# Optimization experiments

Measured on AMD Instinct MI355X. Metric: run time of the kernel, lower is better.

Reference implementation:

```python
import jax, jax.numpy as jnp
import numpy as np

N = 10000
E = 160000
DIMS = [256, 256, 256, 256]
EPS = 1e-5
DSCALE = 1.0
SPE_IDX = 0


def setup_inputs() -> dict:
    key = jax.random.key(0)
    ks = jax.random.split(key, 40)
    inp = {}
    inp['x'] = jax.random.normal(ks[0], (N, DIMS[0]), dtype=jnp.float32)
    inp['src'] = jax.random.randint(ks[1], (E,), 0, N, dtype=jnp.int32)
    inp['dst'] = jax.random.randint(ks[2], (E,), 0, N, dtype=jnp.int32)
    k = 3
    for i, (din, dout) in enumerate(zip(DIMS[:-1], DIMS[1:])):
        s = 1.0 / np.sqrt(din)
        inp[f'Ws{i}'] = jax.random.uniform(ks[k], (din, dout), jnp.float32, -s, s); k += 1
        inp[f'Wn{i}'] = jax.random.uniform(ks[k], (din, dout), jnp.float32, -s, s); k += 1
        inp[f'b{i}'] = jnp.zeros((dout,), jnp.float32)
        inp[f'g{i}'] = jnp.ones((dout,), jnp.float32)
        inp[f'be{i}'] = jnp.zeros((dout,), jnp.float32)
    return inp


def _sage(h, src, dst, Ws, Wn, b):
    # mean aggregation over in-neighbors: segment-sum gathered src feats over dst
    agg = jax.ops.segment_sum(h[src], dst, num_segments=N)          # [N, din]
    deg = jax.ops.segment_sum(jnp.ones((E,), h.dtype), dst, num_segments=N)
    mean = agg / jnp.maximum(deg, 1.0)[:, None]
    return h @ Ws + mean @ Wn + b


def _bn(h, g, be):
    # BatchNorm1d, training mode (biased batch variance)
    mu = jnp.mean(h, axis=0)
    var = jnp.mean((h - mu) ** 2, axis=0)
    return (h - mu) * jax.lax.rsqrt(var + EPS) * g + be


def reference(x, src, dst, Ws0, Wn0, b0, g0, be0, Ws1, Wn1, b1, g1, be1,
              Ws2, Wn2, b2, g2, be2):
    params = [(Ws0, Wn0, b0, g0, be0), (Ws1, Wn1, b1, g1, be1),
              (Ws2, Wn2, b2, g2, be2)]
    n_layers = len(params)
    outs = x
    for i, (Ws, Wn, b, g, be) in enumerate(params):
        outs = _sage(outs, src, dst, Ws, Wn, b)
        # hid side-outputs (sigmoid(outs*dscale)[spe_idx]) don't affect outs path
        outs = _bn(outs, g, be)
        if i != n_layers - 1:
            outs = jax.nn.relu(outs)
        else:
            outs = jax.nn.sigmoid(outs)
    return outs
```

## Files before the change

### kernel.cpp

```cpp
#include <hip/hip_runtime.h>
#include <math.h>

#define NN 10000
#define EE 160000
#define DIM 256
#define KK 512
#define CAP 64
#define EPS_BN 1e-5f
#define AST 516

typedef __attribute__((ext_vector_type(8)))  short bf16x8;
typedef __attribute__((ext_vector_type(16))) float f32x16;

union U16 { uint2 u2[2]; bf16x8 v; };

static __device__ __forceinline__ unsigned short f2bf(float f) {
    unsigned u = __float_as_uint(f);
    unsigned r = (u + 0x7fffu + ((u >> 16) & 1u)) >> 16;
    return (unsigned short)r;
}
static __device__ __forceinline__ float bflo(unsigned v) { return __uint_as_float(v << 16); }
static __device__ __forceinline__ float bfhi(unsigned v) { return __uint_as_float(v & 0xffff0000u); }
static __device__ __forceinline__ unsigned packbf(float a, float b) {
    return (unsigned)f2bf(a) | ((unsigned)f2bf(b) << 16);
}

struct Params {
    const float* x; const int* src; const int* dst;
    const float *Ws0, *Wn0, *Ws1, *Wn1, *Ws2, *Wn2;
    const float *g0, *be0, *g1, *be1, *g2, *be2;
    float* out;
    unsigned short* hx;
    unsigned short* z0;
    unsigned short* z1;
    unsigned short* hn;
    unsigned short* magg;
    unsigned short* wcat;
    float* stats;
    int* cnt;
    int* slots;
};

static __device__ __forceinline__ void accum8(float* a, uint4 v) {
    a[0] += bflo(v.x); a[1] += bfhi(v.x);
    a[2] += bflo(v.y); a[3] += bfhi(v.y);
    a[4] += bflo(v.z); a[5] += bfhi(v.z);
    a[6] += bflo(v.w); a[7] += bfhi(v.w);
}

__global__ __launch_bounds__(256) void k_prep(Params P) {
    int g0 = blockIdx.x * 256 + threadIdx.x;
    int stride = gridDim.x * 256;
    for (int g = g0; g < NN * 64; g += stride) {
        int r = g >> 6, c4 = (g & 63) * 4;
        float4 v = *(const float4*)(P.x + (size_t)r * DIM + c4);
        uint2 p; p.x = packbf(v.x, v.y); p.y = packbf(v.z, v.w);
        *(uint2*)(P.hx + (size_t)r * DIM + c4) = p;
    }
    for (int g = g0; g < 3 * DIM * KK; g += stride) {
        int L = g >> 17; int i = g & 131071;
        int k = i >> 8, n = i & 255;
        const float* Ws = (L == 0) ? P.Ws0 : ((L == 1) ? P.Ws1 : P.Ws2);
        const float* Wn = (L == 0) ? P.Wn0 : ((L == 1) ? P.Wn1 : P.Wn2);
        float v = (k < DIM) ? Ws[(size_t)k * DIM + n] : Wn[(size_t)(k - DIM) * DIM + n];
        P.wcat[(size_t)L * DIM * KK + (size_t)n * KK + k] = f2bf(v);
    }
    for (int g = g0; g < NN + 6 * DIM; g += stride) {
        if (g < NN) P.cnt[g] = 0;
        else P.stats[g - NN] = 0.f;
    }
}

__global__ __launch_bounds__(256) void k_bucket(Params P) {
    int e = blockIdx.x * 256 + threadIdx.x;
    if (e < EE) {
        int d = P.dst[e];
        int p = atomicAdd(&P.cnt[d], 1);
        if (p < CAP) P.slots[(size_t)d * CAP + p] = P.src[e];
    }
}

__global__ __launch_bounds__(256) void k_pre(Params P, int Lprev,
                                             const unsigned short* __restrict__ z,
                                             unsigned short* __restrict__ hn) {
    const float* st  = P.stats + Lprev * 2 * DIM;
    const float* gam = (Lprev == 0) ? P.g0 : P.g1;
    const float* bet = (Lprev == 0) ? P.be0 : P.be1;
    int t = threadIdx.x;
    int c8 = (t & 31) * 8;
    int r = blockIdx.x * 8 + (t >> 5);
    float sc[8], sh[8];
#pragma unroll
    for (int i = 0; i < 8; ++i) {
        int c = c8 + i;
        float mu  = st[c] * (1.0f / NN);
        float var = st[DIM + c] * (1.0f / NN) - mu * mu;
        float k = rsqrtf(var + EPS_BN) * gam[c];
        sc[i] = k;
        sh[i] = bet[c] - mu * k;
    }
    uint4 v = *(const uint4*)(z + (size_t)r * DIM + c8);
    uint4 o;
    o.x = packbf(fmaxf(bflo(v.x) * sc[0] + sh[0], 0.f),
                 fmaxf(bfhi(v.x) * sc[1] + sh[1], 0.f));
    o.y = packbf(fmaxf(bflo(v.y) * sc[2] + sh[2], 0.f),
                 fmaxf(bfhi(v.y) * sc[3] + sh[3], 0.f));
    o.z = packbf(fmaxf(bflo(v.z) * sc[4] + sh[4], 0.f),
                 fmaxf(bfhi(v.z) * sc[5] + sh[5], 0.f));
    o.w = packbf(fmaxf(bflo(v.w) * sc[6] + sh[6], 0.f),
                 fmaxf(bfhi(v.w) * sc[7] + sh[7], 0.f));
    *(uint4*)(hn + (size_t)r * DIM + c8) = o;
}

__global__ __launch_bounds__(256) void k_gather(Params P,
                                                const unsigned short* __restrict__ hsrc,
                                                unsigned short* __restrict__ magg) {
    int t = threadIdx.x;
    int wave = t >> 6, lane = t & 63;
    int h = lane >> 5, l = lane & 31;
    int node = blockIdx.x * 4 + wave;
    if (node >= NN) return;
    int cnt = P.cnt[node]; if (cnt > CAP) cnt = CAP;
    int sv = P.slots[(size_t)node * CAP + lane];
    const uint4* srcm = (const uint4*)hsrc;
    float a[8] = {0, 0, 0, 0, 0, 0, 0, 0};
    int j = 0;
    for (; j + 15 < cnt; j += 16) {
        int r0 = __shfl(sv, j +  0 + h), r1 = __shfl(sv, j +  2 + h);
        int r2 = __shfl(sv, j +  4 + h), r3 = __shfl(sv, j +  6 + h);
        int r4 = __shfl(sv, j +  8 + h), r5 = __shfl(sv, j + 10 + h);
        int r6 = __shfl(sv, j + 12 + h), r7 = __shfl(sv, j + 14 + h);
        uint4 v0 = srcm[(size_t)r0 * 32 + l];
        uint4 v1 = srcm[(size_t)r1 * 32 + l];
        uint4 v2 = srcm[(size_t)r2 * 32 + l];
        uint4 v3 = srcm[(size_t)r3 * 32 + l];
        uint4 v4 = srcm[(size_t)r4 * 32 + l];
        uint4 v5 = srcm[(size_t)r5 * 32 + l];
        uint4 v6 = srcm[(size_t)r6 * 32 + l];
        uint4 v7 = srcm[(size_t)r7 * 32 + l];
        accum8(a, v0); accum8(a, v1); accum8(a, v2); accum8(a, v3);
        accum8(a, v4); accum8(a, v5); accum8(a, v6); accum8(a, v7);
    }
    for (; j + 3 < cnt; j += 4) {
        int r0 = __shfl(sv, j + h), r1 = __shfl(sv, j + 2 + h);
        uint4 v0 = srcm[(size_t)r0 * 32 + l];
        uint4 v1 = srcm[(size_t)r1 * 32 + l];
        accum8(a, v0); accum8(a, v1);
    }
    for (; j + 1 < cnt; j += 2) {
        int r0 = __shfl(sv, j + h);
        uint4 v0 = srcm[(size_t)r0 * 32 + l];
        accum8(a, v0);
    }
    if (j < cnt) {
        int r0 = __shfl(sv, cnt - 1);
        uint4 v0 = srcm[(size_t)r0 * 32 + l];
        if (h == 0) accum8(a, v0);
    }
#pragma unroll
    for (int q = 0; q < 8; ++q) a[q] += __shfl_xor(a[q], 32);
    if (h == 0) {
        float inv = 1.0f / (float)(cnt > 1 ? cnt : 1);
        uint4 o;
        o.x = packbf(a[0] * inv, a[1] * inv);
        o.y = packbf(a[2] * inv, a[3] * inv);
        o.z = packbf(a[4] * inv, a[5] * inv);
        o.w = packbf(a[6] * inv, a[7] * inv);
        ((uint4*)magg)[(size_t)node * 32 + l] = o;
    }
}

__global__ __launch_bounds__(512) void k_gemm(Params P, int L,
                                              const unsigned short* __restrict__ hsrc,
                                              const unsigned short* __restrict__ magg,
                                              unsigned short* __restrict__ gdst) {
    __shared__ unsigned short At[32][AST];
    int t = threadIdx.x;
    int wave = t >> 6, lane = t & 63;
    int h = lane >> 5, l = lane & 31;

    {
        int r = t >> 4, q = t & 15;
        int node = blockIdx.x * 32 + r;
        const unsigned short* srcp = (q < 8) ? hsrc : magg;
        int c0 = (q & 7) * 32;
        unsigned short* dstp = &At[r][(q < 8 ? 0 : 256) + c0];
        if (node < NN) {
            const uint4* gp = (const uint4*)(srcp + (size_t)node * DIM + c0);
            uint4 v0 = gp[0], v1 = gp[1], v2 = gp[2], v3 = gp[3];
            *(uint2*)(dstp)      = make_uint2(v0.x, v0.y);
            *(uint2*)(dstp + 4)  = make_uint2(v0.z, v0.w);
            *(uint2*)(dstp + 8)  = make_uint2(v1.x, v1.y);
            *(uint2*)(dstp + 12) = make_uint2(v1.z, v1.w);
            *(uint2*)(dstp + 16) = make_uint2(v2.x, v2.y);
            *(uint2*)(dstp + 20) = make_uint2(v2.z, v2.w);
            *(uint2*)(dstp + 24) = make_uint2(v3.x, v3.y);
            *(uint2*)(dstp + 28) = make_uint2(v3.z, v3.w);
        } else {
            uint2 z = make_uint2(0u, 0u);
#pragma unroll
            for (int q8 = 0; q8 < 8; ++q8) *(uint2*)(dstp + q8 * 4) = z;
        }
    }
    __syncthreads();

    const unsigned short* wcatL = P.wcat + (size_t)L * DIM * KK;
    float* statsL = P.stats + L * 2 * DIM;
    int m = l;
    int row0 = blockIdx.x * 32;
    int colw0 = wave * 32;
    const unsigned short* Bp = wcatL + (size_t)(colw0 + m) * KK + h * 8;
    const unsigned short* Arow = &At[m][0];
    f32x16 acc;
#pragma unroll
    for (int i = 0; i < 16; ++i) acc[i] = 0.f;
#pragma unroll 8
    for (int k0 = 0; k0 < KK; k0 += 16) {
        U16 ua;
        ua.u2[0] = *(const uint2*)(Arow + k0 + h * 8);
        ua.u2[1] = *(const uint2*)(Arow + k0 + h * 8 + 4);
        bf16x8 av = ua.v;
        bf16x8 bv = *(const bf16x8*)(Bp + k0);
        acc = __builtin_amdgcn_mfma_f32_32x32x16_bf16(av, bv, acc, 0, 0, 0);
    }
    int cc = colw0 + m;
    float s = 0.f, s2 = 0.f;
#pragma unroll
    for (int reg = 0; reg < 16; ++reg) {
        int r = row0 + (reg & 3) + 8 * (reg >> 2) + 4 * h;
        if (r < NN) {
            float v = acc[reg];
            gdst[(size_t)r * DIM + cc] = f2bf(v);
            s += v; s2 += v * v;
        }
    }
    s  += __shfl_down(s, 32);
    s2 += __shfl_down(s2, 32);
    if (h == 0) {
        atomicAdd(&statsL[cc], s);
        atomicAdd(&statsL[DIM + cc], s2);
    }
}

__global__ __launch_bounds__(256) void k_norm(Params P) {
    const float* statsL = P.stats + 2 * 2 * DIM;
    int t = threadIdx.x;
    int c8 = (t & 31) * 8;
    int r = blockIdx.x * 8 + (t >> 5);
    float sc[8], sh[8];
#pragma unroll
    for (int i = 0; i < 8; ++i) {
        int c = c8 + i;
        float mu  = statsL[c] * (1.0f / NN);
        float var = statsL[DIM + c] * (1.0f / NN) - mu * mu;
        float k = rsqrtf(var + EPS_BN) * P.g2[c];
        sc[i] = k;
        sh[i] = P.be2[c] - mu * k;
    }
    uint4 v = *(const uint4*)(P.z0 + (size_t)r * DIM + c8);
    float f[8] = {bflo(v.x), bfhi(v.x), bflo(v.y), bfhi(v.y),
                  bflo(v.z), bfhi(v.z), bflo(v.w), bfhi(v.w)};
#pragma unroll
    for (int i = 0; i < 8; ++i) f[i] = f[i] * sc[i] + sh[i];
    float4 o0, o1;
    o0.x = 1.0f / (1.0f + __expf(-f[0]));
    o0.y = 1.0f / (1.0f + __expf(-f[1]));
    o0.z = 1.0f / (1.0f + __expf(-f[2]));
    o0.w = 1.0f / (1.0f + __expf(-f[3]));
    o1.x = 1.0f / (1.0f + __expf(-f[4]));
    o1.y = 1.0f / (1.0f + __expf(-f[5]));
    o1.z = 1.0f / (1.0f + __expf(-f[6]));
    o1.w = 1.0f / (1.0f + __expf(-f[7]));
    *(float4*)(P.out + (size_t)r * DIM + c8)     = o0;
    *(float4*)(P.out + (size_t)r * DIM + c8 + 4) = o1;
}

extern "C" void kernel_launch(void* const* d_in, const int* in_sizes, int n_in,
                              void* d_out, int out_size, void* d_ws, size_t ws_size,
                              hipStream_t stream) {
    Params P;
    P.x   = (const float*)d_in[0];
    P.src = (const int*)d_in[1];
    P.dst = (const int*)d_in[2];
    P.Ws0 = (const float*)d_in[3];  P.Wn0 = (const float*)d_in[4];
    P.g0  = (const float*)d_in[6];  P.be0 = (const float*)d_in[7];
    P.Ws1 = (const float*)d_in[8];  P.Wn1 = (const float*)d_in[9];
    P.g1  = (const float*)d_in[11]; P.be1 = (const float*)d_in[12];
    P.Ws2 = (const float*)d_in[13]; P.Wn2 = (const float*)d_in[14];
    P.g2  = (const float*)d_in[16]; P.be2 = (const float*)d_in[17];
    P.out = (float*)d_out;

    char* ws = (char*)d_ws;
    size_t off = 0;
    P.hx   = (unsigned short*)(ws + off); off += (size_t)NN * DIM * 2;
    P.z0   = (unsigned short*)(ws + off); off += (size_t)NN * DIM * 2;
    P.z1   = (unsigned short*)(ws + off); off += (size_t)NN * DIM * 2;
    P.hn   = (unsigned short*)(ws + off); off += (size_t)NN * DIM * 2;
    P.magg = (unsigned short*)(ws + off); off += (size_t)NN * DIM * 2;
    P.wcat = (unsigned short*)(ws + off); off += (size_t)3 * DIM * KK * 2;
    P.stats = (float*)(ws + off); off += 3 * 2 * DIM * sizeof(float);
    P.cnt   = (int*)(ws + off); off += (size_t)NN * 4; off = (off + 255) & ~(size_t)255;
    P.slots = (int*)(ws + off); off += (size_t)NN * CAP * 4;
    (void)ws_size;

    k_prep<<<512, 256, 0, stream>>>(P);
    k_bucket<<<(EE + 255) / 256, 256, 0, stream>>>(P);
    k_gather<<<2500, 256, 0, stream>>>(P, P.hx, P.magg);
    k_gemm<<<313, 512, 0, stream>>>(P, 0, P.hx, P.magg, P.z0);
    k_pre<<<1250, 256, 0, stream>>>(P, 0, P.z0, P.hn);
    k_gather<<<2500, 256, 0, stream>>>(P, P.hn, P.magg);
    k_gemm<<<313, 512, 0, stream>>>(P, 1, P.hn, P.magg, P.z1);
    k_pre<<<1250, 256, 0, stream>>>(P, 1, P.z1, P.hn);
    k_gather<<<2500, 256, 0, stream>>>(P, P.hn, P.magg);
    k_gemm<<<313, 512, 0, stream>>>(P, 2, P.hn, P.magg, P.z0);
    k_norm<<<NN / 8, 256, 0, stream>>>(P);
}
```

Measured before the change: 220.0 us.

## Split gather feature columns across two blocks, four edges per wave iteration

Each node's 256-wide bf16 feature row is now split into two halves handled by different blocks. Each wave processes four neighbor edges at once in 16-lane groups instead of two edges in 32-lane groups. The grid doubles, and block IDs are interleaved so that both halves of a node group launch close together. This aims to expose more independent gathers and memory parallelism per wave for the mean aggregation, at the cost of duplicated slot and count loads and an extra shuffle-reduction step.

```diff
diff --git a/kernel.cpp b/kernel.cpp
--- a/kernel.cpp
+++ b/kernel.cpp
@@ -117,56 +117,54 @@
                                                 unsigned short* __restrict__ magg) {
     int t = threadIdx.x;
     int wave = t >> 6, lane = t & 63;
-    int h = lane >> 5, l = lane & 31;
-    int node = blockIdx.x * 4 + wave;
+    int g16 = lane >> 4, l16 = lane & 15;
+    int bid = blockIdx.x;
+    int half = (bid >> 2) & 1;
+    int grp  = (bid >> 3) * 4 + (bid & 3);
+    int node = grp * 4 + wave;
     if (node >= NN) return;
     int cnt = P.cnt[node]; if (cnt > CAP) cnt = CAP;
     int sv = P.slots[(size_t)node * CAP + lane];
     const uint4* srcm = (const uint4*)hsrc;
+    int cbase = half * 16 + l16;
     float a[8] = {0, 0, 0, 0, 0, 0, 0, 0};
     int j = 0;
     for (; j + 15 < cnt; j += 16) {
-        int r0 = __shfl(sv, j +  0 + h), r1 = __shfl(sv, j +  2 + h);
-        int r2 = __shfl(sv, j +  4 + h), r3 = __shfl(sv, j +  6 + h);
-        int r4 = __shfl(sv, j +  8 + h), r5 = __shfl(sv, j + 10 + h);
-        int r6 = __shfl(sv, j + 12 + h), r7 = __shfl(sv, j + 14 + h);
-        uint4 v0 = srcm[(size_t)r0 * 32 + l];
-        uint4 v1 = srcm[(size_t)r1 * 32 + l];
-        uint4 v2 = srcm[(size_t)r2 * 32 + l];
-        uint4 v3 = srcm[(size_t)r3 * 32 + l];
-        uint4 v4 = srcm[(size_t)r4 * 32 + l];
-        uint4 v5 = srcm[(size_t)r5 * 32 + l];
-        uint4 v6 = srcm[(size_t)r6 * 32 + l];
-        uint4 v7 = srcm[(size_t)r7 * 32 + l];
+        int r0 = __shfl(sv, j +  0 + g16);
+        int r1 = __shfl(sv, j +  4 + g16);
+        int r2 = __shfl(sv, j +  8 + g16);
+        int r3 = __shfl(sv, j + 12 + g16);
+        uint4 v0 = srcm[(size_t)r0 * 32 + cbase];
+        uint4 v1 = srcm[(size_t)r1 * 32 + cbase];
+        uint4 v2 = srcm[(size_t)r2 * 32 + cbase];
+        uint4 v3 = srcm[(size_t)r3 * 32 + cbase];
         accum8(a, v0); accum8(a, v1); accum8(a, v2); accum8(a, v3);
-        accum8(a, v4); accum8(a, v5); accum8(a, v6); accum8(a, v7);
     }
     for (; j + 3 < cnt; j += 4) {
-        int r0 = __shfl(sv, j + h), r1 = __shfl(sv, j + 2 + h);
-        uint4 v0 = srcm[(size_t)r0 * 32 + l];
-        uint4 v1 = srcm[(size_t)r1 * 32 + l];
-        accum8(a, v0); accum8(a, v1);
-    }
-    for (; j + 1 < cnt; j += 2) {
-        int r0 = __shfl(sv, j + h);
-        uint4 v0 = srcm[(size_t)r0 * 32 + l];
+        int r0 = __shfl(sv, j + g16);
+        uint4 v0 = srcm[(size_t)r0 * 32 + cbase];
         accum8(a, v0);
     }
     if (j < cnt) {
-        int r0 = __shfl(sv, cnt - 1);
-        uint4 v0 = srcm[(size_t)r0 * 32 + l];
-        if (h == 0) accum8(a, v0);
-    }
-#pragma unroll
-    for (int q = 0; q < 8; ++q) a[q] += __shfl_xor(a[q], 32);
-    if (h == 0) {
+        int jj = j + g16;
+        int jc = (jj < cnt) ? jj : j;
+        int r0 = __shfl(sv, jc);
+        uint4 v0 = srcm[(size_t)r0 * 32 + cbase];
+        if (jj < cnt) accum8(a, v0);
+    }
+#pragma unroll
+    for (int q = 0; q < 8; ++q) {
+        a[q] += __shfl_xor(a[q], 16);
+        a[q] += __shfl_xor(a[q], 32);
+    }
+    if (g16 == 0) {
         float inv = 1.0f / (float)(cnt > 1 ? cnt : 1);
         uint4 o;
         o.x = packbf(a[0] * inv, a[1] * inv);
         o.y = packbf(a[2] * inv, a[3] * inv);
         o.z = packbf(a[4] * inv, a[5] * inv);
         o.w = packbf(a[6] * inv, a[7] * inv);
-        ((uint4*)magg)[(size_t)node * 32 + l] = o;
+        ((uint4*)magg)[(size_t)node * 32 + cbase] = o;
     }
 }
 
@@ -305,13 +303,13 @@
 
     k_prep<<<512, 256, 0, stream>>>(P);
     k_bucket<<<(EE + 255) / 256, 256, 0, stream>>>(P);
-    k_gather<<<2500, 256, 0, stream>>>(P, P.hx, P.magg);
+    k_gather<<<5000, 256, 0, stream>>>(P, P.hx, P.magg);
     k_gemm<<<313, 512, 0, stream>>>(P, 0, P.hx, P.magg, P.z0);
     k_pre<<<1250, 256, 0, stream>>>(P, 0, P.z0, P.hn);
-    k_gather<<<2500, 256, 0, stream>>>(P, P.hn, P.magg);
+    k_gather<<<5000, 256, 0, stream>>>(P, P.hn, P.magg);
     k_gemm<<<313, 512, 0, stream>>>(P, 1, P.hn, P.magg, P.z1);
     k_pre<<<1250, 256, 0, stream>>>(P, 1, P.z1, P.hn);
-    k_gather<<<2500, 256, 0, stream>>>(P, P.hn, P.magg);
+    k_gather<<<5000, 256, 0, stream>>>(P, P.hn, P.magg);
     k_gemm<<<313, 512, 0, stream>>>(P, 2, P.hn, P.magg, P.z0);
     k_norm<<<NN / 8, 256, 0, stream>>>(P);
 }
```

Result: no change. 220.9 us (+0.4%).

## Fuse all GraphSAGE layers into one cooperative persistent kernel with grid syncs

Applied to the files above, without the earlier changes.

Replaces the eleven-kernel launch chain with a single cooperative kernel that runs prep, bucketing, gather, GEMM and final norm, separated by grid-wide syncs. The previous layer's BatchNorm and ReLU are now applied on the fly during the gather and when the GEMM A tile is loaded, so the separate pre-normalization pass and its intermediate buffer are gone. The aim is to cut launch gaps and one full read/write of activations per layer. In exchange, the GEMM runs on a grid of 256 or 512 blocks instead of 313, normalization arithmetic is recomputed for every gathered edge, and grid-sync costs are added. The old multi-kernel path remains as a fallback if the cooperative launch fails.

```diff
diff --git a/kernel.cpp b/kernel.cpp
--- a/kernel.cpp
+++ b/kernel.cpp
@@ -1,5 +1,8 @@
 #include <hip/hip_runtime.h>
+#include <hip/hip_cooperative_groups.h>
 #include <math.h>
+
+namespace cg = cooperative_groups;
 
 #define NN 10000
 #define EE 160000
@@ -8,6 +11,7 @@
 #define CAP 64
 #define EPS_BN 1e-5f
 #define AST 516
+#define BLK 512
 
 typedef __attribute__((ext_vector_type(8)))  short bf16x8;
 typedef __attribute__((ext_vector_type(16))) float f32x16;
@@ -46,6 +50,255 @@
     a[2] += bflo(v.y); a[3] += bfhi(v.y);
     a[4] += bflo(v.z); a[5] += bfhi(v.z);
     a[6] += bflo(v.w); a[7] += bfhi(v.w);
+}
+static __device__ __forceinline__ void accum8n(float* a, uint4 v,
+                                               const float* sc, const float* sh) {
+    a[0] += fmaxf(bflo(v.x) * sc[0] + sh[0], 0.f);
+    a[1] += fmaxf(bfhi(v.x) * sc[1] + sh[1], 0.f);
+    a[2] += fmaxf(bflo(v.y) * sc[2] + sh[2], 0.f);
+    a[3] += fmaxf(bfhi(v.y) * sc[3] + sh[3], 0.f);
+    a[4] += fmaxf(bflo(v.z) * sc[4] + sh[4], 0.f);
+    a[5] += fmaxf(bfhi(v.z) * sc[5] + sh[5], 0.f);
+    a[6] += fmaxf(bflo(v.w) * sc[6] + sh[6], 0.f);
+    a[7] += fmaxf(bfhi(v.w) * sc[7] + sh[7], 0.f);
+}
+
+__global__ __launch_bounds__(BLK, 4) void k_mega(Params P) {
+    cg::grid_group grid = cg::this_grid();
+    __shared__ unsigned short At[32][AST];
+    const int t = threadIdx.x;
+    const int bid = blockIdx.x;
+    const int nblk = gridDim.x;
+    const int gtid = bid * BLK + t;
+    const int gstride = nblk * BLK;
+    const int wave = t >> 6, lane = t & 63;
+    const int h = lane >> 5, l = lane & 31;
+
+    for (int g = gtid; g < NN * 64; g += gstride) {
+        int r = g >> 6, c4 = (g & 63) * 4;
+        float4 v = *(const float4*)(P.x + (size_t)r * DIM + c4);
+        uint2 p; p.x = packbf(v.x, v.y); p.y = packbf(v.z, v.w);
+        *(uint2*)(P.hx + (size_t)r * DIM + c4) = p;
+    }
+    for (int g = gtid; g < 3 * DIM * KK; g += gstride) {
+        int L = g >> 17; int i = g & 131071;
+        int k = i >> 8, n = i & 255;
+        const float* Ws = (L == 0) ? P.Ws0 : ((L == 1) ? P.Ws1 : P.Ws2);
+        const float* Wn = (L == 0) ? P.Wn0 : ((L == 1) ? P.Wn1 : P.Wn2);
+        float v = (k < DIM) ? Ws[(size_t)k * DIM + n] : Wn[(size_t)(k - DIM) * DIM + n];
+        P.wcat[(size_t)L * DIM * KK + (size_t)n * KK + k] = f2bf(v);
+    }
+    for (int g = gtid; g < NN + 6 * DIM; g += gstride) {
+        if (g < NN) P.cnt[g] = 0;
+        else P.stats[g - NN] = 0.f;
+    }
+    grid.sync();
+
+    for (int e = gtid; e < EE; e += gstride) {
+        int d = P.dst[e];
+        int p = atomicAdd(&P.cnt[d], 1);
+        if (p < CAP) P.slots[(size_t)d * CAP + p] = P.src[e];
+    }
+    grid.sync();
+
+    for (int L = 0; L < 3; ++L) {
+        const unsigned short* src = (L == 0) ? P.hx : ((L == 1) ? P.z0 : P.z1);
+        unsigned short* dst = (L == 0) ? P.z0 : ((L == 1) ? P.z1 : P.z0);
+        const float* gam = (L == 1) ? P.g0 : P.g1;
+        const float* bet = (L == 1) ? P.be0 : P.be1;
+        const float* stp = P.stats + (L - 1) * 2 * DIM;
+
+        float sc[8], sh[8];
+        if (L > 0) {
+#pragma unroll
+            for (int i = 0; i < 8; ++i) {
+                int c = l * 8 + i;
+                float mu  = stp[c] * (1.0f / NN);
+                float var = stp[DIM + c] * (1.0f / NN) - mu * mu;
+                float k = rsqrtf(var + EPS_BN) * gam[c];
+                sc[i] = k;
+                sh[i] = bet[c] - mu * k;
+            }
+        }
+
+        {
+            const uint4* srcm = (const uint4*)src;
+            int wid = bid * 8 + wave;
+            for (int node = wid; node < NN; node += nblk * 8) {
+                int cnt = P.cnt[node]; if (cnt > CAP) cnt = CAP;
+                int sv = P.slots[(size_t)node * CAP + lane];
+                float a[8] = {0, 0, 0, 0, 0, 0, 0, 0};
+                int j = 0;
+                for (; j + 15 < cnt; j += 16) {
+                    int r0 = __shfl(sv, j +  0 + h), r1 = __shfl(sv, j +  2 + h);
+                    int r2 = __shfl(sv, j +  4 + h), r3 = __shfl(sv, j +  6 + h);
+                    int r4 = __shfl(sv, j +  8 + h), r5 = __shfl(sv, j + 10 + h);
+                    int r6 = __shfl(sv, j + 12 + h), r7 = __shfl(sv, j + 14 + h);
+                    uint4 v0 = srcm[(size_t)r0 * 32 + l];
+                    uint4 v1 = srcm[(size_t)r1 * 32 + l];
+                    uint4 v2 = srcm[(size_t)r2 * 32 + l];
+                    uint4 v3 = srcm[(size_t)r3 * 32 + l];
+                    uint4 v4 = srcm[(size_t)r4 * 32 + l];
+                    uint4 v5 = srcm[(size_t)r5 * 32 + l];
+                    uint4 v6 = srcm[(size_t)r6 * 32 + l];
+                    uint4 v7 = srcm[(size_t)r7 * 32 + l];
+                    if (L == 0) {
+                        accum8(a, v0); accum8(a, v1); accum8(a, v2); accum8(a, v3);
+                        accum8(a, v4); accum8(a, v5); accum8(a, v6); accum8(a, v7);
+                    } else {
+                        accum8n(a, v0, sc, sh); accum8n(a, v1, sc, sh);
+                        accum8n(a, v2, sc, sh); accum8n(a, v3, sc, sh);
+                        accum8n(a, v4, sc, sh); accum8n(a, v5, sc, sh);
+                        accum8n(a, v6, sc, sh); accum8n(a, v7, sc, sh);
+                    }
+                }
+                for (; j + 3 < cnt; j += 4) {
+                    int r0 = __shfl(sv, j + h), r1 = __shfl(sv, j + 2 + h);
+                    uint4 v0 = srcm[(size_t)r0 * 32 + l];
+                    uint4 v1 = srcm[(size_t)r1 * 32 + l];
+                    if (L == 0) { accum8(a, v0); accum8(a, v1); }
+                    else { accum8n(a, v0, sc, sh); accum8n(a, v1, sc, sh); }
+                }
+                for (; j + 1 < cnt; j += 2) {
+                    int r0 = __shfl(sv, j + h);
+                    uint4 v0 = srcm[(size_t)r0 * 32 + l];
+                    if (L == 0) accum8(a, v0); else accum8n(a, v0, sc, sh);
+                }
+                if (j < cnt) {
+                    int r0 = __shfl(sv, cnt - 1);
+                    uint4 v0 = srcm[(size_t)r0 * 32 + l];
+                    if (h == 0) {
+                        if (L == 0) accum8(a, v0); else accum8n(a, v0, sc, sh);
+                    }
+                }
+#pragma unroll
+                for (int q = 0; q < 8; ++q) a[q] += __shfl_xor(a[q], 32);
+                if (h == 0) {
+                    float inv = 1.0f / (float)(cnt > 1 ? cnt : 1);
+                    uint4 o;
+                    o.x = packbf(a[0] * inv, a[1] * inv);
+                    o.y = packbf(a[2] * inv, a[3] * inv);
+                    o.z = packbf(a[4] * inv, a[5] * inv);
+                    o.w = packbf(a[6] * inv, a[7] * inv);
+                    ((uint4*)P.magg)[(size_t)node * 32 + l] = o;
+                }
+            }
+        }
+        grid.sync();
+
+        {
+            int cgS = t & 31, rs = t >> 5;
+            float scg[8], shg[8];
+            if (L > 0) {
+#pragma unroll
+                for (int i = 0; i < 8; ++i) {
+                    int c = cgS * 8 + i;
+                    float mu  = stp[c] * (1.0f / NN);
+                    float var = stp[DIM + c] * (1.0f / NN) - mu * mu;
+                    float k = rsqrtf(var + EPS_BN) * gam[c];
+                    scg[i] = k;
+                    shg[i] = bet[c] - mu * k;
+                }
+            }
+            const unsigned short* wcatL = P.wcat + (size_t)L * DIM * KK;
+            float* statsL = P.stats + L * 2 * DIM;
+            for (int tile = bid; tile < 313; tile += nblk) {
+#pragma unroll
+                for (int rr = 0; rr < 2; ++rr) {
+                    int r = rs + rr * 16;
+                    int node = tile * 32 + r;
+                    unsigned short* arow = &At[r][0];
+                    if (node < NN) {
+                        uint4 ov = *(const uint4*)(src + (size_t)node * DIM + cgS * 8);
+                        if (L > 0) {
+                            uint4 o;
+                            o.x = packbf(fmaxf(bflo(ov.x) * scg[0] + shg[0], 0.f),
+                                         fmaxf(bfhi(ov.x) * scg[1] + shg[1], 0.f));
+                            o.y = packbf(fmaxf(bflo(ov.y) * scg[2] + shg[2], 0.f),
+                                         fmaxf(bfhi(ov.y) * scg[3] + shg[3], 0.f));
+                            o.z = packbf(fmaxf(bflo(ov.z) * scg[4] + shg[4], 0.f),
+                                         fmaxf(bfhi(ov.z) * scg[5] + shg[5], 0.f));
+                            o.w = packbf(fmaxf(bflo(ov.w) * scg[6] + shg[6], 0.f),
+                                         fmaxf(bfhi(ov.w) * scg[7] + shg[7], 0.f));
+                            ov = o;
+                        }
+                        *(uint2*)(arow + cgS * 8)     = make_uint2(ov.x, ov.y);
+                        *(uint2*)(arow + cgS * 8 + 4) = make_uint2(ov.z, ov.w);
+                        uint4 mv = *(const uint4*)(P.magg + (size_t)node * DIM + cgS * 8);
+                        *(uint2*)(arow + 256 + cgS * 8)     = make_uint2(mv.x, mv.y);
+                        *(uint2*)(arow + 256 + cgS * 8 + 4) = make_uint2(mv.z, mv.w);
+                    } else {
+                        uint2 z2 = make_uint2(0u, 0u);
+                        *(uint2*)(arow + cgS * 8)           = z2;
+                        *(uint2*)(arow + cgS * 8 + 4)       = z2;
+                        *(uint2*)(arow + 256 + cgS * 8)     = z2;
+                        *(uint2*)(arow + 256 + cgS * 8 + 4) = z2;
+                    }
+                }
+                __syncthreads();
+                int m = l;
+                int row0 = tile * 32;
+                int colw0 = wave * 32;
+                const unsigned short* Bp = wcatL + (size_t)(colw0 + m) * KK + h * 8;
+                const unsigned short* Arow = &At[m][0];
+                f32x16 acc;
+#pragma unroll
+                for (int i = 0; i < 16; ++i) acc[i] = 0.f;
+#pragma unroll 8
+                for (int k0 = 0; k0 < KK; k0 += 16) {
+                    U16 ua;
+                    ua.u2[0] = *(const uint2*)(Arow + k0 + h * 8);
+                    ua.u2[1] = *(const uint2*)(Arow + k0 + h * 8 + 4);
+                    bf16x8 av = ua.v;
+                    bf16x8 bv = *(const bf16x8*)(Bp + k0);
+                    acc = __builtin_amdgcn_mfma_f32_32x32x16_bf16(av, bv, acc, 0, 0, 0);
+                }
+                int cc = colw0 + m;
+                float s = 0.f, s2 = 0.f;
+#pragma unroll
+                for (int reg = 0; reg < 16; ++reg) {
+                    int r = row0 + (reg & 3) + 8 * (reg >> 2) + 4 * h;
+                    if (r < NN) {
+                        float v = acc[reg];
+                        dst[(size_t)r * DIM + cc] = f2bf(v);
+                        s += v; s2 += v * v;
+                    }
+                }
+                s  += __shfl_down(s, 32);
+                s2 += __shfl_down(s2, 32);
+                if (h == 0) {
+                    atomicAdd(&statsL[cc], s);
+                    atomicAdd(&statsL[DIM + cc], s2);
+                }
+                __syncthreads();
+            }
+        }
+        grid.sync();
+    }
+
+    {
+        const float* statsL = P.stats + 2 * 2 * DIM;
+        for (int g = gtid; g < NN * 32; g += gstride) {
+            int r = g >> 5, c8 = (g & 31) * 8;
+            float f[8];
+            uint4 v = *(const uint4*)(P.z0 + (size_t)r * DIM + c8);
+            f[0] = bflo(v.x); f[1] = bfhi(v.x); f[2] = bflo(v.y); f[3] = bfhi(v.y);
+            f[4] = bflo(v.z); f[5] = bfhi(v.z); f[6] = bflo(v.w); f[7] = bfhi(v.w);
+#pragma unroll
+            for (int i = 0; i < 8; ++i) {
+                int c = c8 + i;
+                float mu  = statsL[c] * (1.0f / NN);
+                float var = statsL[DIM + c] * (1.0f / NN) - mu * mu;
+                float k = rsqrtf(var + EPS_BN) * P.g2[c];
+                float z = f[i] * k + (P.be2[c] - mu * k);
+                f[i] = 1.0f / (1.0f + __expf(-z));
+            }
+            float4 o0 = make_float4(f[0], f[1], f[2], f[3]);
+            float4 o1 = make_float4(f[4], f[5], f[6], f[7]);
+            *(float4*)(P.out + (size_t)r * DIM + c8)     = o0;
+            *(float4*)(P.out + (size_t)r * DIM + c8 + 4) = o1;
+        }
+    }
 }
 
 __global__ __launch_bounds__(256) void k_prep(Params P) {
@@ -178,7 +431,6 @@
     int t = threadIdx.x;
     int wave = t >> 6, lane = t & 63;
     int h = lane >> 5, l = lane & 31;
-
     {
         int r = t >> 4, q = t & 15;
         int node = blockIdx.x * 32 + r;
@@ -203,7 +455,6 @@
         }
     }
     __syncthreads();
-
     const unsigned short* wcatL = P.wcat + (size_t)L * DIM * KK;
     float* statsL = P.stats + L * 2 * DIM;
     int m = l;
@@ -303,15 +554,33 @@
     P.slots = (int*)(ws + off); off += (size_t)NN * CAP * 4;
     (void)ws_size;
 
-    k_prep<<<512, 256, 0, stream>>>(P);
-    k_bucket<<<(EE + 255) / 256, 256, 0, stream>>>(P);
-    k_gather<<<2500, 256, 0, stream>>>(P, P.hx, P.magg);
-    k_gemm<<<313, 512, 0, stream>>>(P, 0, P.hx, P.magg, P.z0);
-    k_pre<<<1250, 256, 0, stream>>>(P, 0, P.z0, P.hn);
-    k_gather<<<2500, 256, 0, stream>>>(P, P.hn, P.magg);
-    k_gemm<<<313, 512, 0, stream>>>(P, 1, P.hn, P.magg, P.z1);
-    k_pre<<<1250, 256, 0, stream>>>(P, 1, P.z1, P.hn);
-    k_gather<<<2500, 256, 0, stream>>>(P, P.hn, P.magg);
-    k_gemm<<<313, 512, 0, stream>>>(P, 2, P.hn, P.magg, P.z0);
-    k_norm<<<NN / 8, 256, 0, stream>>>(P);
-}
+    static int coop_grid = -1;
+    if (coop_grid < 0) {
+        int occ = 0;
+        hipError_t e = hipOccupancyMaxActiveBlocksPerMultiprocessor(&occ, k_mega, BLK, 0);
+        if (e != hipSuccess || occ < 1) { coop_grid = 0; (void)hipGetLastError(); }
+        else coop_grid = (occ >= 2) ? 512 : 256;
+    }
+
+    bool done = false;
+    if (coop_grid > 0) {
+        void* kargs[] = { (void*)&P };
+        hipError_t e = hipLaunchCooperativeKernel(k_mega, dim3(coop_grid), dim3(BLK),
+                                                  kargs, 0, stream);
+        if (e == hipSuccess) done = true;
+        else { (void)hipGetLastError(); coop_grid = 0; }
+    }
+    if (!done) {
+        k_prep<<<512, 256, 0, stream>>>(P);
+        k_bucket<<<(EE + 255) / 256, 256, 0, stream>>>(P);
+        k_gather<<<2500, 256, 0, stream>>>(P, P.hx, P.magg);
+        k_gemm<<<313, 512, 0, stream>>>(P, 0, P.hx, P.magg, P.z0);
+        k_pre<<<1250, 256, 0, stream>>>(P, 0, P.z0, P.hn);
+        k_gather<<<2500, 256, 0, stream>>>(P, P.hn, P.magg);
+        k_gemm<<<313, 512, 0, stream>>>(P, 1, P.hn, P.magg, P.z1);
+        k_pre<<<1250, 256, 0, stream>>>(P, 1, P.z1, P.hn);
+        k_gather<<<2500, 256, 0, stream>>>(P, P.hn, P.magg);
+        k_gemm<<<313, 512, 0, stream>>>(P, 2, P.hn, P.magg, P.z0);
+        k_norm<<<NN / 8, 256, 0, stream>>>(P);
+    }
+}
```

Measured after the change: 552.0 us. 2.51x slower.
